# Performance work log

Hardware: AMD Instinct MI355X
Metric: run time of the kernel (lower is better)

## Reference

```python
import jax, jax.numpy as jnp
import numpy as np

EMBED_DIM = 1024
NUM_HEADS = 16
HEAD_DIM = EMBED_DIM // NUM_HEADS


def setup_inputs() -> dict:
    key = jax.random.key(0)
    k1, k2, k3, k4 = jax.random.split(key, 4)
    B, S, D = 2, 2048, EMBED_DIM
    x = jax.random.normal(k1, (B, S, D), dtype=jnp.float32)
    xpos = jax.random.randint(k2, (B, S), 0, 2048, dtype=jnp.int32)
    # torch nn.Linear weights: [out_features, in_features]; qkv_bias=False -> no qkv bias
    qkv_w = jax.random.normal(k3, (3 * D, D), dtype=jnp.float32) * (D ** -0.5)
    proj_w = jax.random.normal(k4, (D, D), dtype=jnp.float32) * (D ** -0.5)
    proj_b = jnp.zeros((D,), dtype=jnp.float32)
    return {"x": x, "xpos": xpos, "qkv_w": qkv_w, "proj_w": proj_w, "proj_b": proj_b}


def reference(x, xpos, qkv_w, proj_w, proj_b):
    # rope is None, dropout rates are 0, so xpos is unused and dropout is identity.
    B, S, D = x.shape
    H, hd = NUM_HEADS, D // NUM_HEADS
    scale = hd ** -0.5

    qkv = x @ qkv_w.T                                   # [B, S, 3D]
    qkv = qkv.reshape(B, S, 3, H, hd)
    qkv = jnp.transpose(qkv, (0, 3, 2, 1, 4))           # [B, H, 3, S, hd]
    q, k, v = qkv[:, :, 0], qkv[:, :, 1], qkv[:, :, 2]  # each [B, H, S, hd]

    scores = jnp.einsum("bhqd,bhkd->bhqk", q, k) * scale  # [B, H, S, S]
    probs = jax.nn.softmax(scores, axis=-1)
    out = jnp.einsum("bhqk,bhkd->bhqd", probs, v)         # [B, H, S, hd]

    out = jnp.transpose(out, (0, 2, 1, 3)).reshape(B, S, D)
    out = out @ proj_w.T + proj_b
    return out
```

## Files before the change

kernel.cpp:

```cpp
#include <hip/hip_runtime.h>


typedef __bf16 bf16_8 __attribute__((ext_vector_type(8)));
typedef __bf16 bf16_4 __attribute__((ext_vector_type(4)));
typedef __bf16 bf16_2 __attribute__((ext_vector_type(2)));
typedef float floatx4 __attribute__((ext_vector_type(4)));

#define MFMA16 __builtin_amdgcn_mfma_f32_16x16x32_bf16
#define CSCALE 0.1803368801111204f
#define EXP2R  __builtin_amdgcn_exp2f

__device__ __forceinline__ void gld16(const __bf16* g, __bf16* l) {
    __builtin_amdgcn_global_load_lds(
        (const __attribute__((address_space(1))) void*)g,
        (__attribute__((address_space(3))) void*)l, 16, 0, 0);
}

__device__ __forceinline__ unsigned pk_bf16(float a, float b) {
    bf16_2 t;
    t[0] = (__bf16)a; t[1] = (__bf16)b;
    return __builtin_bit_cast(unsigned, t);
}

__global__ __launch_bounds__(256) void cvt_all(
    const float* __restrict__ x, const float* __restrict__ w1,
    const float* __restrict__ w2,
    __bf16* __restrict__ xb, __bf16* __restrict__ w1b, __bf16* __restrict__ w2b)
{
    const int i = blockIdx.x * 256 + threadIdx.x;
    const float* src; __bf16* dst; int off;
    if (i < (1 << 20))                  { src = x;  dst = xb;  off = i; }
    else if (i < (1 << 20) + 786432)    { src = w1; dst = w1b; off = i - (1 << 20); }
    else                                { src = w2; dst = w2b; off = i - (1 << 20) - 786432; }
    float4 v = ((const float4*)src)[off];
    bf16_4 o;
    o[0] = (__bf16)v.x; o[1] = (__bf16)v.y; o[2] = (__bf16)v.z; o[3] = (__bf16)v.w;
    ((bf16_4*)dst)[off] = o;
}

__device__ __forceinline__ void gemm_bt_mainloop(
    const __bf16* __restrict__ A, const __bf16* __restrict__ B,
    int K, __bf16* As, __bf16* Bs, floatx4 (&acc)[4][4])
{
    const int tid  = threadIdx.x;
    const int lane = tid & 63;
    const int wv   = tid >> 6;
    const int quad = lane >> 4;
    const int l15  = lane & 15;
    const int wm   = (wv >> 1) * 64;
    const int wn   = (wv & 1) * 64;

    for (int k0 = 0; k0 < K; k0 += 64) {
        __syncthreads();
#pragma unroll
        for (int it = 0; it < 4; ++it) {
            int cc = it * 256 + tid;
            int row = cc >> 3, kc = cc & 7;
            gld16(A + row * K + k0 + ((kc ^ (row & 7)) * 8), &As[cc * 8]);
        }
#pragma unroll
        for (int it = 0; it < 4; ++it) {
            int cc = it * 256 + tid;
            int row = cc >> 3, kc = cc & 7;
            gld16(B + row * K + k0 + ((kc ^ (row & 7)) * 8), &Bs[cc * 8]);
        }
        __syncthreads();

#pragma unroll
        for (int ks = 0; ks < 2; ++ks) {
            bf16_8 af[4], bf[4];
#pragma unroll
            for (int mt = 0; mt < 4; ++mt) {
                int r = wm + mt * 16 + l15;
                af[mt] = *(const bf16_8*)&As[r * 64 + (((ks * 4 + quad) ^ (r & 7)) * 8)];
            }
#pragma unroll
            for (int nt = 0; nt < 4; ++nt) {
                int r = wn + nt * 16 + l15;
                bf[nt] = *(const bf16_8*)&Bs[r * 64 + (((ks * 4 + quad) ^ (r & 7)) * 8)];
            }
#pragma unroll
            for (int mt = 0; mt < 4; ++mt)
#pragma unroll
                for (int nt = 0; nt < 4; ++nt)
                    acc[mt][nt] = MFMA16(af[mt], bf[nt], acc[mt][nt], 0, 0, 0);
        }
    }
}

__global__ __launch_bounds__(256) void qkv_gemm(
    const __bf16* __restrict__ X, const __bf16* __restrict__ W,
    __bf16* __restrict__ q_ws, __bf16* __restrict__ k_ws, __bf16* __restrict__ vt_ws)
{
    __shared__ __align__(16) __bf16 As[128 * 64];
    __shared__ __align__(16) __bf16 Bs[128 * 64];
    floatx4 acc[4][4] = {};
    const int m0 = blockIdx.y * 128, n0 = blockIdx.x * 128;
    const int c = n0 >> 10;

    const int tid = threadIdx.x, lane = tid & 63, wv = tid >> 6;
    const int quad = lane >> 4, l15 = lane & 15;
    const int wm = (wv >> 1) * 64, wn = (wv & 1) * 64;

    if (c == 2) {
        gemm_bt_mainloop(X + (size_t)m0 * 1024, W + (size_t)n0 * 1024, 1024, As, Bs, acc);
#pragma unroll
        for (int mt = 0; mt < 4; ++mt) {
            const int mbase = m0 + wm + mt * 16 + quad * 4;
            const int b = mbase >> 11, s = mbase & 2047;
#pragma unroll
            for (int nt = 0; nt < 4; ++nt) {
                const int n = n0 + wn + nt * 16 + l15;
                const int h = (n >> 6) & 15, d = n & 63;
                bf16_4 pk;
#pragma unroll
                for (int r = 0; r < 4; ++r) pk[r] = (__bf16)acc[mt][nt][r];
                *(bf16_4*)&vt_ws[((b * 16 + h) * 64 + d) * 2048 + s] = pk;
            }
        }
    } else {
        gemm_bt_mainloop(W + (size_t)n0 * 1024, X + (size_t)m0 * 1024, 1024, As, Bs, acc);
        __bf16* dst = (c == 0) ? q_ws : k_ws;
        const float scale = (c == 1) ? CSCALE : 1.0f;
#pragma unroll
        for (int mt = 0; mt < 4; ++mt) {
            const int nn = n0 + wm + mt * 16 + quad * 4;
            const int h = (nn >> 6) & 15, d0 = nn & 63;
#pragma unroll
            for (int nt = 0; nt < 4; ++nt) {
                const int token = m0 + wn + nt * 16 + l15;
                const int b = token >> 11, s = token & 2047;
                bf16_4 pk;
#pragma unroll
                for (int r = 0; r < 4; ++r) pk[r] = (__bf16)(acc[mt][nt][r] * scale);
                *(bf16_4*)&dst[((b * 16 + h) * 2048 + s) * 64 + d0] = pk;
            }
        }
    }
}

__global__ __launch_bounds__(512) void attn_kernel(
    const __bf16* __restrict__ q_ws, const __bf16* __restrict__ k_ws,
    const __bf16* __restrict__ vt_ws, __bf16* __restrict__ attn_ws)
{
    __shared__ __align__(16) __bf16 Ks [2][64 * 64];
    __shared__ __align__(16) __bf16 Vts[2][64 * 64];
    __shared__ __align__(16) __bf16 Ps [8][2][16][72];

    const int tid = threadIdx.x, lane = tid & 63, w = tid >> 6;
    const int half = tid >> 8, htid = tid & 255, wh = w & 3;
    const int quad = lane >> 4, l15 = lane & 15;
    const int bh = blockIdx.x, qt = blockIdx.y;
    const int q0 = qt * 128;
    const int koff = half * 1024;

    const __bf16* qp  = q_ws  + (size_t)bh * (2048 * 64);
    const __bf16* kp  = k_ws  + (size_t)bh * (2048 * 64);
    const __bf16* vtp = vt_ws + (size_t)bh * (64 * 2048);

    const int srow = htid >> 3, skc = htid & 7;
    const int sw   = (skc ^ (srow & 7)) * 8;
    const __bf16* kb0 = kp  + (size_t)(koff + srow) * 64 + sw;
    const __bf16* kb1 = kp  + (size_t)(koff + srow + 32) * 64 + sw;
    const __bf16* vb0 = vtp + (size_t)srow * 2048 + koff + sw;
    const __bf16* vb1 = vtp + (size_t)(srow + 32) * 2048 + koff + sw;
    const int ldsoff = (srow * 8 + skc) * 8;

    bf16_8 qf[2][2];
#pragma unroll
    for (int qg = 0; qg < 2; ++qg) {
        const int qrow = q0 + wh * 32 + qg * 16 + l15;
        qf[qg][0] = *(const bf16_8*)&qp[qrow * 64 + quad * 8];
        qf[qg][1] = *(const bf16_8*)&qp[qrow * 64 + 32 + quad * 8];
    }

    bf16_8 ones;
#pragma unroll
    for (int j = 0; j < 8; ++j) ones[j] = (__bf16)1.0f;

    floatx4 oacc[2][4] = {};
    floatx4 lsum[2] = {};

#pragma unroll 1
    for (int kt = 0; kt < 16; ++kt) {
        const int ko = kt * 64;
        __syncthreads();
        gld16(kb0 + ko * 64, &Ks[half][ldsoff]);
        gld16(kb1 + ko * 64, &Ks[half][ldsoff + 2048]);
        gld16(vb0 + ko,      &Vts[half][ldsoff]);
        gld16(vb1 + ko,      &Vts[half][ldsoff + 2048]);
        __syncthreads();

        const __bf16* Kb = Ks[half];
        const __bf16* Vb = Vts[half];

        floatx4 sacc[2][4] = {};
#pragma unroll
        for (int ks = 0; ks < 2; ++ks)
#pragma unroll
            for (int kg = 0; kg < 4; ++kg) {
                int krow = kg * 16 + l15;
                bf16_8 kf = *(const bf16_8*)&Kb[krow * 64 + (((ks * 4 + quad) ^ (krow & 7)) * 8)];
                sacc[0][kg] = MFMA16(kf, qf[0][ks], sacc[0][kg], 0, 0, 0);
                sacc[1][kg] = MFMA16(kf, qf[1][ks], sacc[1][kg], 0, 0, 0);
            }

#pragma unroll
        for (int qg = 0; qg < 2; ++qg)
#pragma unroll
            for (int kg = 0; kg < 4; ++kg) {
                uint2 pk;
                pk.x = pk_bf16(EXP2R(sacc[qg][kg][0]), EXP2R(sacc[qg][kg][1]));
                pk.y = pk_bf16(EXP2R(sacc[qg][kg][2]), EXP2R(sacc[qg][kg][3]));
                *(uint2*)&Ps[w][qg][l15][kg * 16 + quad * 4] = pk;
            }
        __asm__ __volatile__("s_waitcnt lgkmcnt(0)" ::: "memory");

#pragma unroll
        for (int ks = 0; ks < 2; ++ks) {
            bf16_8 pf0 = *(const bf16_8*)&Ps[w][0][l15][ks * 32 + quad * 8];
            bf16_8 pf1 = *(const bf16_8*)&Ps[w][1][l15][ks * 32 + quad * 8];
            lsum[0] = MFMA16(ones, pf0, lsum[0], 0, 0, 0);
            lsum[1] = MFMA16(ones, pf1, lsum[1], 0, 0, 0);
#pragma unroll
            for (int dg = 0; dg < 4; ++dg) {
                int drow = dg * 16 + l15;
                bf16_8 vf = *(const bf16_8*)&Vb[drow * 64 + (((ks * 4 + quad) ^ (drow & 7)) * 8)];
                oacc[0][dg] = MFMA16(vf, pf0, oacc[0][dg], 0, 0, 0);
                oacc[1][dg] = MFMA16(vf, pf1, oacc[1][dg], 0, 0, 0);
            }
        }
    }

    __syncthreads();
    float* comb  = (float*)Ps;
    float* lcomb = comb + 128 * 68;
    if (half == 1) {
#pragma unroll
        for (int qg = 0; qg < 2; ++qg) {
            const int q = wh * 32 + qg * 16 + l15;
#pragma unroll
            for (int dg = 0; dg < 4; ++dg)
                *(floatx4*)&comb[q * 68 + dg * 16 + quad * 4] = oacc[qg][dg];
            if (quad == 0) lcomb[q] = lsum[qg][0];
        }
    }
    __syncthreads();
    if (half == 0) {
        const int b = bh >> 4, h = bh & 15;
#pragma unroll
        for (int qg = 0; qg < 2; ++qg) {
            const int q = wh * 32 + qg * 16 + l15;
            const float inv_l = 1.0f / (lsum[qg][0] + lcomb[q]);
            const int token = b * 2048 + q0 + q;
#pragma unroll
            for (int dg = 0; dg < 4; ++dg) {
                floatx4 v2 = *(const floatx4*)&comb[q * 68 + dg * 16 + quad * 4];
                bf16_4 ok;
#pragma unroll
                for (int r = 0; r < 4; ++r)
                    ok[r] = (__bf16)((oacc[qg][dg][r] + v2[r]) * inv_l);
                *(bf16_4*)&attn_ws[(size_t)token * 1024 + h * 64 + dg * 16 + quad * 4] = ok;
            }
        }
    }
}

__global__ __launch_bounds__(256) void proj_gemm(
    const __bf16* __restrict__ Ain, const __bf16* __restrict__ W,
    const float* __restrict__ bias, float* __restrict__ out)
{
    __shared__ __align__(16) __bf16 As[128 * 64];
    __shared__ __align__(16) __bf16 Bs[64 * 64];
    floatx4 acc[4][2] = {};
    const int m0 = blockIdx.y * 128, n0 = blockIdx.x * 64;

    const int tid = threadIdx.x, lane = tid & 63, wv = tid >> 6;
    const int quad = lane >> 4, l15 = lane & 15;
    const int wm = (wv >> 1) * 64, wn = (wv & 1) * 32;

    const __bf16* A  = Ain + (size_t)m0 * 1024;
    const __bf16* Bp = W   + (size_t)n0 * 1024;

    for (int k0 = 0; k0 < 1024; k0 += 64) {
        __syncthreads();
#pragma unroll
        for (int it = 0; it < 4; ++it) {
            int cc = it * 256 + tid;
            int row = cc >> 3, kc = cc & 7;
            gld16(A + row * 1024 + k0 + ((kc ^ (row & 7)) * 8), &As[cc * 8]);
        }
#pragma unroll
        for (int it = 0; it < 2; ++it) {
            int cc = it * 256 + tid;
            int row = cc >> 3, kc = cc & 7;
            gld16(Bp + row * 1024 + k0 + ((kc ^ (row & 7)) * 8), &Bs[cc * 8]);
        }
        __syncthreads();

#pragma unroll
        for (int ks = 0; ks < 2; ++ks) {
            bf16_8 af[4], bf[2];
#pragma unroll
            for (int mt = 0; mt < 4; ++mt) {
                int r = wm + mt * 16 + l15;
                af[mt] = *(const bf16_8*)&As[r * 64 + (((ks * 4 + quad) ^ (r & 7)) * 8)];
            }
#pragma unroll
            for (int nt = 0; nt < 2; ++nt) {
                int r = wn + nt * 16 + l15;
                bf[nt] = *(const bf16_8*)&Bs[r * 64 + (((ks * 4 + quad) ^ (r & 7)) * 8)];
            }
#pragma unroll
            for (int mt = 0; mt < 4; ++mt)
#pragma unroll
                for (int nt = 0; nt < 2; ++nt)
                    acc[mt][nt] = MFMA16(af[mt], bf[nt], acc[mt][nt], 0, 0, 0);
        }
    }

    float bv[2];
#pragma unroll
    for (int nt = 0; nt < 2; ++nt) bv[nt] = bias[n0 + wn + nt * 16 + l15];

#pragma unroll
    for (int mt = 0; mt < 4; ++mt) {
        const int m = m0 + wm + mt * 16 + quad * 4;
#pragma unroll
        for (int nt = 0; nt < 2; ++nt) {
            const int n = n0 + wn + nt * 16 + l15;
#pragma unroll
            for (int r = 0; r < 4; ++r)
                out[(size_t)(m + r) * 1024 + n] = acc[mt][nt][r] + bv[nt];
        }
    }
}

extern "C" void kernel_launch(void* const* d_in, const int* in_sizes, int n_in,
                              void* d_out, int out_size, void* d_ws, size_t ws_size,
                              hipStream_t stream)
{
    const float* x      = (const float*)d_in[0];
    const float* qkv_w  = (const float*)d_in[2];
    const float* proj_w = (const float*)d_in[3];
    const float* proj_b = (const float*)d_in[4];
    float* out = (float*)d_out;

    const size_t SZ   = 4096 * 1024;
    const size_t WQKV = 3072 * 1024;
    const size_t WPRJ = 1024 * 1024;

    __bf16* xb      = (__bf16*)d_ws;
    __bf16* qkvwb   = xb + SZ;
    __bf16* projwb  = qkvwb + WQKV;
    __bf16* q_ws    = projwb + WPRJ;
    __bf16* k_ws    = q_ws + SZ;
    __bf16* vt_ws   = k_ws + SZ;
    __bf16* attn_ws = vt_ws + SZ;

    cvt_all<<<dim3(8192), 256, 0, stream>>>(x, qkv_w, proj_w, xb, qkvwb, projwb);
    qkv_gemm  <<<dim3(24, 32), 256, 0, stream>>>(xb, qkvwb, q_ws, k_ws, vt_ws);
    attn_kernel<<<dim3(32, 16), 512, 0, stream>>>(q_ws, k_ws, vt_ws, attn_ws);
    proj_gemm <<<dim3(16, 32), 256, 0, stream>>>(attn_ws, projwb, proj_b, out);
}
```

Before: 184.1 us.

## Split QKV GEMM K dimension across two intra-block halves with LDS reduction

The QKV projection kernel now runs 512 threads per block. Each 256-thread half computes the same 128x128 output tile over half of the K range, using its own LDS buffers. The second half writes its accumulators to shared memory, and the first half adds them before the epilogue. This doubles the waves per tile, aiming to hide the latency of the serial, unpipelined K loop. The cost is double the LDS per block, an extra reduction pass through shared memory, and half the threads sitting idle during the epilogue.

Result: faster. 176.6 us (-4.1%).

```diff
diff --git a/kernel.cpp b/kernel.cpp
--- a/kernel.cpp
+++ b/kernel.cpp
@@ -38,31 +38,44 @@
     ((bf16_4*)dst)[off] = o;
 }
 
-__device__ __forceinline__ void gemm_bt_mainloop(
-    const __bf16* __restrict__ A, const __bf16* __restrict__ B,
-    int K, __bf16* As, __bf16* Bs, floatx4 (&acc)[4][4])
-{
-    const int tid  = threadIdx.x;
-    const int lane = tid & 63;
-    const int wv   = tid >> 6;
-    const int quad = lane >> 4;
-    const int l15  = lane & 15;
-    const int wm   = (wv >> 1) * 64;
-    const int wn   = (wv & 1) * 64;
-
-    for (int k0 = 0; k0 < K; k0 += 64) {
+__global__ __launch_bounds__(512) void qkv_gemm(
+    const __bf16* __restrict__ X, const __bf16* __restrict__ W,
+    __bf16* __restrict__ q_ws, __bf16* __restrict__ k_ws, __bf16* __restrict__ vt_ws)
+{
+    __shared__ __align__(16) __bf16 S[2][2][128 * 64];
+
+    const int tid = threadIdx.x, lane = tid & 63;
+    const int half = tid >> 8, htid = tid & 255;
+    const int wvh = (tid >> 6) & 3;
+    const int quad = lane >> 4, l15 = lane & 15;
+    const int wm = (wvh >> 1) * 64, wn = (wvh & 1) * 64;
+    const int m0 = blockIdx.y * 128, n0 = blockIdx.x * 128;
+    const int c = n0 >> 10;
+
+    const __bf16* Abase;
+    const __bf16* Bbase;
+    if (c == 2) { Abase = X + (size_t)m0 * 1024; Bbase = W + (size_t)n0 * 1024; }
+    else        { Abase = W + (size_t)n0 * 1024; Bbase = X + (size_t)m0 * 1024; }
+    Abase += half * 512;
+    Bbase += half * 512;
+
+    __bf16* As = S[half][0];
+    __bf16* Bs = S[half][1];
+    floatx4 acc[4][4] = {};
+
+    for (int k0 = 0; k0 < 512; k0 += 64) {
         __syncthreads();
 #pragma unroll
         for (int it = 0; it < 4; ++it) {
-            int cc = it * 256 + tid;
+            int cc = it * 256 + htid;
             int row = cc >> 3, kc = cc & 7;
-            gld16(A + row * K + k0 + ((kc ^ (row & 7)) * 8), &As[cc * 8]);
+            gld16(Abase + row * 1024 + k0 + ((kc ^ (row & 7)) * 8), &As[cc * 8]);
         }
 #pragma unroll
         for (int it = 0; it < 4; ++it) {
-            int cc = it * 256 + tid;
+            int cc = it * 256 + htid;
             int row = cc >> 3, kc = cc & 7;
-            gld16(B + row * K + k0 + ((kc ^ (row & 7)) * 8), &Bs[cc * 8]);
+            gld16(Bbase + row * 1024 + k0 + ((kc ^ (row & 7)) * 8), &Bs[cc * 8]);
         }
         __syncthreads();
 
@@ -86,24 +99,26 @@
                     acc[mt][nt] = MFMA16(af[mt], bf[nt], acc[mt][nt], 0, 0, 0);
         }
     }
-}
-
-__global__ __launch_bounds__(256) void qkv_gemm(
-    const __bf16* __restrict__ X, const __bf16* __restrict__ W,
-    __bf16* __restrict__ q_ws, __bf16* __restrict__ k_ws, __bf16* __restrict__ vt_ws)
-{
-    __shared__ __align__(16) __bf16 As[128 * 64];
-    __shared__ __align__(16) __bf16 Bs[128 * 64];
-    floatx4 acc[4][4] = {};
-    const int m0 = blockIdx.y * 128, n0 = blockIdx.x * 128;
-    const int c = n0 >> 10;
-
-    const int tid = threadIdx.x, lane = tid & 63, wv = tid >> 6;
-    const int quad = lane >> 4, l15 = lane & 15;
-    const int wm = (wv >> 1) * 64, wn = (wv & 1) * 64;
+
+    __syncthreads();
+    float* comb = (float*)S;
+    if (half == 1) {
+#pragma unroll
+        for (int mt = 0; mt < 4; ++mt)
+#pragma unroll
+            for (int nt = 0; nt < 4; ++nt)
+                *(floatx4*)&comb[((mt * 4 + nt) * 256 + htid) * 4] = acc[mt][nt];
+    }
+    __syncthreads();
+    if (half != 0) return;
+
+#pragma unroll
+    for (int mt = 0; mt < 4; ++mt)
+#pragma unroll
+        for (int nt = 0; nt < 4; ++nt)
+            acc[mt][nt] += *(const floatx4*)&comb[((mt * 4 + nt) * 256 + htid) * 4];
 
     if (c == 2) {
-        gemm_bt_mainloop(X + (size_t)m0 * 1024, W + (size_t)n0 * 1024, 1024, As, Bs, acc);
 #pragma unroll
         for (int mt = 0; mt < 4; ++mt) {
             const int mbase = m0 + wm + mt * 16 + quad * 4;
@@ -119,7 +134,6 @@
             }
         }
     } else {
-        gemm_bt_mainloop(W + (size_t)n0 * 1024, X + (size_t)m0 * 1024, 1024, As, Bs, acc);
         __bf16* dst = (c == 0) ? q_ws : k_ws;
         const float scale = (c == 1) ? CSCALE : 1.0f;
 #pragma unroll
@@ -359,7 +373,7 @@
     __bf16* attn_ws = vt_ws + SZ;
 
     cvt_all<<<dim3(8192), 256, 0, stream>>>(x, qkv_w, proj_w, xb, qkvwb, projwb);
-    qkv_gemm  <<<dim3(24, 32), 256, 0, stream>>>(xb, qkvwb, q_ws, k_ws, vt_ws);
+    qkv_gemm  <<<dim3(24, 32), 512, 0, stream>>>(xb, qkvwb, q_ws, k_ws, vt_ws);
     attn_kernel<<<dim3(32, 16), 512, 0, stream>>>(q_ws, k_ws, vt_ws, attn_ws);
     proj_gemm <<<dim3(16, 32), 256, 0, stream>>>(attn_ws, projwb, proj_b, out);
 }
```
